# Performance work log

Hardware: AMD Instinct MI355X
Metric: run time of the kernel (lower is better)

Reference implementation:

```python
import jax, jax.numpy as jnp
import numpy as np


def build_edge_index(num_nodes: int, height: int, width: int) -> np.ndarray:
    """Vectorized, order-faithful reproduction of EdgeIndexGenerator.forward.

    Per node i (in order): [i,i], then (if present) left pair, right pair,
    up pair, down pair. After the loop, the torch code (block is OUTSIDE the
    loop) appends one symmetric pair for the last node only.
    Returns int64 array of shape [2, E].
    """
    N, H, W = num_nodes, height, width
    HW = H * W
    ids = np.arange(N, dtype=np.int64)
    b = ids // HW
    p = ids % HW
    x = p % W
    y = p // W

    # 9 candidate rows per node: self, left x2, right x2, up x2, down x2
    rows = np.zeros((N, 9, 2), dtype=np.int64)
    mask = np.zeros((N, 9), dtype=bool)

    rows[:, 0, 0] = ids; rows[:, 0, 1] = ids; mask[:, 0] = True

    left = b * HW + y * W + (x - 1)
    m = x > 0
    rows[:, 1, 0] = ids; rows[:, 1, 1] = left
    rows[:, 2, 0] = left; rows[:, 2, 1] = ids
    mask[:, 1] = m; mask[:, 2] = m

    right = b * HW + y * W + (x + 1)
    m = x < W - 1
    rows[:, 3, 0] = ids; rows[:, 3, 1] = right
    rows[:, 4, 0] = right; rows[:, 4, 1] = ids
    mask[:, 3] = m; mask[:, 4] = m

    up = b * HW + (y - 1) * W + x
    m = y > 0
    rows[:, 5, 0] = ids; rows[:, 5, 1] = up
    rows[:, 6, 0] = up; rows[:, 6, 1] = ids
    mask[:, 5] = m; mask[:, 6] = m

    down = b * HW + (y + 1) * W + x
    m = y < H - 1
    rows[:, 7, 0] = ids; rows[:, 7, 1] = down
    rows[:, 8, 0] = down; rows[:, 8, 1] = ids
    mask[:, 7] = m; mask[:, 8] = m

    edges = rows.reshape(N * 9, 2)[mask.reshape(-1)]

    # symmetric pair for LAST node only (loop-variable leak in original code)
    i = N - 1
    cx = (W - 1) / 2
    cy = (H - 1) / 2
    sx = int(2 * cx - x[-1])
    sy = int(2 * cy - y[-1])
    sidx = int(b[-1]) * HW + sy * W + sx
    if sidx != i:
        edges = np.concatenate([edges, np.array([[i, sidx], [sidx, i]], dtype=np.int64)], axis=0)
    return edges.T  # [2, E]


def setup_inputs() -> dict:
    key = jax.random.key(0)
    B, H, W, C = 64, 56, 56, 256
    node_features = jax.random.normal(key, (B * H * W, C), dtype=jnp.float32)
    return {"node_features": node_features, "height": H, "width": W}


def reference(node_features, height, width):
    num_nodes = node_features.shape[0]  # only the size is used, as in torch
    edge_index = build_edge_index(num_nodes, height, width)  # static shapes
    return jnp.asarray(edge_index)  # [2, E] int64 (int32 on default jax)
```

## Files before the change

### kernel.cpp

```cpp
#include <hip/hip_runtime.h>


__global__ void __launch_bounds__(256)
EdgeIndexGenerator_12524124635757_kernel(
        const int* __restrict__ hptr, const int* __restrict__ wptr,
        int* __restrict__ out, unsigned int outSize) {
    const unsigned int H = (unsigned int)*hptr;
    const unsigned int W = (unsigned int)*wptr;
    const unsigned int E = outSize >> 1;
    const unsigned int HW = H * W;
    const unsigned int perBatch = HW + 4u * H * (W - 1) + 4u * W * (H - 1);
    const unsigned int B = E / perBatch;
    const unsigned int rem = E - B * perBatch;
    const unsigned int N = B * HW;

    const unsigned int stride = gridDim.x * blockDim.x;
    for (unsigned int i = blockIdx.x * blockDim.x + threadIdx.x; i < N; i += stride) {
        const unsigned int b = i / HW;
        const unsigned int p = i - b * HW;
        const unsigned int x = p % W;
        const unsigned int y = p / W;

        const unsigned int ry = (y > 0) + (y < H - 1);
        const unsigned int rowsPrefix =
            y * (3u * W + 4u * (W - 1)) + 2u * W * (y > 0 ? y - 1 : 0);
        const unsigned int sumRow =
            x * (1u + 2u * ry) + 2u * ((x > 0 ? x - 1 : 0) + x);
        unsigned int o = b * perBatch + rowsPrefix + sumRow;

        const int ii = (int)i;
        out[o] = ii; out[E + o] = ii; ++o;
        if (x > 0) {
            const int n = ii - 1;
            out[o] = ii; out[E + o] = n; ++o;
            out[o] = n;  out[E + o] = ii; ++o;
        }
        if (x < W - 1) {
            const int n = ii + 1;
            out[o] = ii; out[E + o] = n; ++o;
            out[o] = n;  out[E + o] = ii; ++o;
        }
        if (y > 0) {
            const int n = ii - (int)W;
            out[o] = ii; out[E + o] = n; ++o;
            out[o] = n;  out[E + o] = ii; ++o;
        }
        if (y < H - 1) {
            const int n = ii + (int)W;
            out[o] = ii; out[E + o] = n; ++o;
            out[o] = n;  out[E + o] = ii; ++o;
        }

        if (rem == 2 && i == N - 1) {
            const int sx = (int)(W - 1 - x);
            const int sy = (int)(H - 1 - y);
            const int sidx = (int)(b * HW) + sy * (int)W + sx;
            out[E - 2]     = ii;   out[E - 1]     = sidx;
            out[2 * E - 2] = sidx; out[2 * E - 1] = ii;
        }
    }
}

extern "C" void kernel_launch(void* const* d_in, const int* in_sizes, int n_in,
                              void* d_out, int out_size, void* d_ws, size_t ws_size,
                              hipStream_t stream) {
    const int* hptr = (const int*)d_in[1];
    const int* wptr = (const int*)d_in[2];
    int* out = (int*)d_out;

    const int threads = 256;
    const int blocks = 1024;
    EdgeIndexGenerator_12524124635757_kernel<<<blocks, threads, 0, stream>>>(
        hptr, wptr, out, (unsigned int)out_size);
}
```

Before: 245.0 us.

## Stage per-chunk edge rows in shared memory for coalesced global stores

Each block now handles a chunk of 256 nodes, writes each node's variable-length edge entries into two shared-memory arrays at local offsets, then copies the contiguous span to global memory with coalesced, thread-strided stores. Previously each thread wrote its own scattered run of up to 9 entries directly to global memory, giving uncoalesced writes. The cost is two block barriers per chunk and extra offset computation for the chunk bounds. The shared buffers are sized for the worst case of 9 entries per node.

```diff
diff --git a/kernel.cpp b/kernel.cpp
--- a/kernel.cpp
+++ b/kernel.cpp
@@ -1,5 +1,29 @@
 #include <hip/hip_runtime.h>
 
+
+__device__ __forceinline__ unsigned int node_off(
+        unsigned int i, unsigned int HW, unsigned int W, unsigned int H,
+        unsigned int perBatch) {
+    const unsigned int b = i / HW;
+    const unsigned int p = i - b * HW;
+    const unsigned int y = p / W;
+    const unsigned int x = p - y * W;
+    const unsigned int ry = (y > 0) + (y < H - 1);
+    const unsigned int rowsPrefix =
+        y * (3u * W + 4u * (W - 1)) + 2u * W * (y > 0 ? y - 1 : 0);
+    const unsigned int sumRow =
+        x * (1u + 2u * ry) + 2u * ((x > 0 ? x - 1 : 0) + x);
+    return b * perBatch + rowsPrefix + sumRow;
+}
+
+__device__ __forceinline__ unsigned int node_cnt(
+        unsigned int i, unsigned int HW, unsigned int W, unsigned int H) {
+    const unsigned int b = i / HW;
+    const unsigned int p = i - b * HW;
+    const unsigned int y = p / W;
+    const unsigned int x = p - y * W;
+    return 1u + 2u * ((x > 0) + (x < W - 1) + (y > 0) + (y < H - 1));
+}
 
 __global__ void __launch_bounds__(256)
 EdgeIndexGenerator_12524124635757_kernel(
@@ -14,50 +38,70 @@
     const unsigned int rem = E - B * perBatch;
     const unsigned int N = B * HW;
 
-    const unsigned int stride = gridDim.x * blockDim.x;
-    for (unsigned int i = blockIdx.x * blockDim.x + threadIdx.x; i < N; i += stride) {
-        const unsigned int b = i / HW;
-        const unsigned int p = i - b * HW;
-        const unsigned int x = p % W;
-        const unsigned int y = p / W;
+    __shared__ int s0[2304];
+    __shared__ int s1[2304];
 
-        const unsigned int ry = (y > 0) + (y < H - 1);
-        const unsigned int rowsPrefix =
-            y * (3u * W + 4u * (W - 1)) + 2u * W * (y > 0 ? y - 1 : 0);
-        const unsigned int sumRow =
-            x * (1u + 2u * ry) + 2u * ((x > 0 ? x - 1 : 0) + x);
-        unsigned int o = b * perBatch + rowsPrefix + sumRow;
+    const unsigned int nChunks = (N + 255u) >> 8;
+    for (unsigned int chunk = blockIdx.x; chunk < nChunks; chunk += gridDim.x) {
+        const unsigned int i0 = chunk << 8;
+        const unsigned int iLast = (i0 + 255u < N - 1u) ? (i0 + 255u) : (N - 1u);
 
-        const int ii = (int)i;
-        out[o] = ii; out[E + o] = ii; ++o;
-        if (x > 0) {
-            const int n = ii - 1;
-            out[o] = ii; out[E + o] = n; ++o;
-            out[o] = n;  out[E + o] = ii; ++o;
+        const unsigned int base = node_off(i0, HW, W, H, perBatch);
+        const unsigned int span =
+            node_off(iLast, HW, W, H, perBatch) + node_cnt(iLast, HW, W, H) - base;
+
+        const unsigned int i = i0 + threadIdx.x;
+        if (i <= iLast) {
+            const unsigned int b = i / HW;
+            const unsigned int p = i - b * HW;
+            const unsigned int y = p / W;
+            const unsigned int x = p - y * W;
+            unsigned int lo = node_off(i, HW, W, H, perBatch) - base;
+
+            const int ii = (int)i;
+            s0[lo] = ii; s1[lo] = ii; ++lo;
+            if (x > 0) {
+                const int n = ii - 1;
+                s0[lo] = ii; s1[lo] = n;  ++lo;
+                s0[lo] = n;  s1[lo] = ii; ++lo;
+            }
+            if (x < W - 1) {
+                const int n = ii + 1;
+                s0[lo] = ii; s1[lo] = n;  ++lo;
+                s0[lo] = n;  s1[lo] = ii; ++lo;
+            }
+            if (y > 0) {
+                const int n = ii - (int)W;
+                s0[lo] = ii; s1[lo] = n;  ++lo;
+                s0[lo] = n;  s1[lo] = ii; ++lo;
+            }
+            if (y < H - 1) {
+                const int n = ii + (int)W;
+                s0[lo] = ii; s1[lo] = n;  ++lo;
+                s0[lo] = n;  s1[lo] = ii; ++lo;
+            }
         }
-        if (x < W - 1) {
-            const int n = ii + 1;
-            out[o] = ii; out[E + o] = n; ++o;
-            out[o] = n;  out[E + o] = ii; ++o;
-        }
-        if (y > 0) {
-            const int n = ii - (int)W;
-            out[o] = ii; out[E + o] = n; ++o;
-            out[o] = n;  out[E + o] = ii; ++o;
-        }
-        if (y < H - 1) {
-            const int n = ii + (int)W;
-            out[o] = ii; out[E + o] = n; ++o;
-            out[o] = n;  out[E + o] = ii; ++o;
+        __syncthreads();
+
+        for (unsigned int t = threadIdx.x; t < span; t += 256u) {
+            out[base + t]     = s0[t];
+            out[E + base + t] = s1[t];
         }
 
-        if (rem == 2 && i == N - 1) {
-            const int sx = (int)(W - 1 - x);
-            const int sy = (int)(H - 1 - y);
+        if (rem == 2u && i == N - 1u) {
+            const unsigned int b = i / HW;
+            const unsigned int p = i - b * HW;
+            const unsigned int y = p / W;
+            const unsigned int x = p - y * W;
+            const int ii = (int)i;
+            const int sx = (int)(W - 1u - x);
+            const int sy = (int)(H - 1u - y);
             const int sidx = (int)(b * HW) + sy * (int)W + sx;
-            out[E - 2]     = ii;   out[E - 1]     = sidx;
-            out[2 * E - 2] = sidx; out[2 * E - 1] = ii;
+            out[E - 2u]      = ii;   out[E - 1u]      = sidx;
+            out[2u * E - 2u] = sidx; out[2u * E - 1u] = ii;
         }
+
+        __syncthreads();
     }
 }
 
```

Result: faster. 235.6 us (-3.8%).
